# Optimization experiments

Hardware: AMD Instinct MI355X
Metric: run time of the kernel (lower is better)

Reference implementation:

```python
import jax, jax.numpy as jnp
import numpy as np

B, C, H, W = 2, 256, 48, 64
NLVL, NHEAD, D1 = 4, 8, 32


def _avg_pool2(x):
    b, c, h, w = x.shape
    return x.reshape(b, c, h // 2, 2, w // 2, 2).mean(axis=(3, 5))


def _grid_sample(img, grid):
    """Bilinear grid_sample, align_corners=False, zeros padding.
    img: [B,C,Hi,Wi], grid: [B,Hg,Wg,2] in [-1,1]. Returns [B,C,Hg,Wg]."""
    _, _, Hi, Wi = img.shape
    x = (grid[..., 0] + 1.0) * 0.5 * Wi - 0.5
    y = (grid[..., 1] + 1.0) * 0.5 * Hi - 0.5
    x0 = jnp.floor(x)
    y0 = jnp.floor(y)
    wx1 = x - x0
    wx0 = 1.0 - wx1
    wy1 = y - y0
    wy0 = 1.0 - wy1

    def corner(xi, yi, wgt):
        valid = (xi >= 0) & (xi <= Wi - 1) & (yi >= 0) & (yi <= Hi - 1)
        xc = jnp.clip(xi, 0, Wi - 1).astype(jnp.int32)
        yc = jnp.clip(yi, 0, Hi - 1).astype(jnp.int32)
        v = jax.vmap(lambda im, yy, xx: im[:, yy, xx])(img, yc, xc)  # [B,C,Hg,Wg]
        return v * (wgt * valid)[:, None]

    return (corner(x0, y0, wx0 * wy0) + corner(x0 + 1, y0, wx1 * wy0)
            + corner(x0, y0 + 1, wx0 * wy1) + corner(x0 + 1, y0 + 1, wx1 * wy1))


def _forward(fmap1, fmap2, coords, num_levels, num_head):
    batch, _, n1, d1, h1, w1 = coords.shape
    # pyramid from fmap2 (register)
    pyr = [fmap2]
    f2 = fmap2
    for _ in range(num_levels - 1):
        f2 = _avg_pool2(f2)
        pyr.append(f2)
    c = jnp.transpose(coords, (2, 0, 4, 5, 3, 1)).reshape(num_levels, batch, h1 * w1, d1, 2)
    f1 = fmap1[..., None]  # [B,C,h1,w1,1]
    outs = []
    for i in range(num_levels):
        coord = c[i]
        xg = 2.0 * (coord[..., 0] + 0.5) / w1 - 1.0
        yg = 2.0 * (coord[..., 1] + 0.5) / h1 - 1.0
        grid = jnp.stack([xg, yg], axis=-1)  # [B, h1*w1, d1, 2]
        s = _grid_sample(pyr[i], grid)  # [B, C, h1*w1, d1]
        s = s.reshape(batch, -1, h1, w1, d1)
        corr = jnp.abs(f1 - s)  # [B,C,h1,w1,d1]
        corr = corr.reshape(batch, num_head, -1, h1, w1, d1).mean(axis=2)  # [B,nh,h1,w1,d1]
        corr = jnp.transpose(corr, (0, 2, 3, 1, 4)).reshape(batch, h1, w1, -1)
        outs.append(corr)
    out = jnp.concatenate(outs, axis=-1)  # [B,h1,w1,nlvl*nh*d1]
    return jnp.transpose(out, (0, 3, 1, 2)).astype(jnp.float32)


def setup_inputs() -> dict:
    key = jax.random.key(0)
    k1, k2, k3 = jax.random.split(key, 3)
    fmap1 = jax.random.normal(k1, (B, C, H, W), dtype=jnp.float32)
    fmap2 = jax.random.normal(k2, (B, C, H, W), dtype=jnp.float32)
    # coords in fmap1 pixel units: x in [0,W), y in [0,H)
    u = jax.random.uniform(k3, (B, 2, NLVL, D1, H, W), dtype=jnp.float32)
    scale = jnp.array([W, H], dtype=jnp.float32).reshape(1, 2, 1, 1, 1, 1)
    coords = u * scale
    return {"fmap1": fmap1, "fmap2": fmap2, "coords": coords,
            "num_levels": NLVL, "num_head": NHEAD}


def reference(fmap1, fmap2, coords, num_levels, num_head):
    return _forward(fmap1, fmap2, coords, num_levels, num_head)
```

## Files before the change

### kernel.cpp

```cpp
#include <hip/hip_runtime.h>

typedef _Float16 h2 __attribute__((ext_vector_type(2)));

static constexpr int B2   = 2;
static constexpr int C    = 256;
static constexpr int H    = 48;
static constexpr int W    = 64;
static constexpr int NLVL = 4;
static constexpr int D1   = 32;
static constexpr int P    = H * W;
static constexpr int CHO  = NLVL * 8 * D1;

static constexpr size_t F1_BYTES = (size_t)B2 * P * C * 2;
static constexpr size_t PL0 = 0;
static constexpr size_t PL1 = PL0 + (size_t)B2 * 48 * 64 * C;
static constexpr size_t PL2 = PL1 + (size_t)B2 * 24 * 32 * C;
static constexpr size_t PL3 = PL2 + (size_t)B2 * 12 * 16 * C;
static constexpr size_t PYR_BYTES = PL3 + (size_t)B2 * 6 * 8 * C;
static constexpr size_t OT_OFF    = F1_BYTES + PYR_BYTES;
static constexpr size_t OT_BYTES  = (size_t)B2 * P * CHO * 2;
static constexpr size_t WS_NEEDED = OT_OFF + OT_BYTES;

#if defined(__has_builtin)
#if __has_builtin(__builtin_amdgcn_cvt_scalef32_pk_f16_fp8)
#define HAS_HW_FP8_DEC 1
#endif
#if __has_builtin(__builtin_amdgcn_cvt_pk_fp8_f32)
#define HAS_HW_FP8_ENC 1
#endif
#endif

#ifdef HAS_HW_FP8_DEC
static constexpr float WSC = 1.0f;
#else
static constexpr float WSC = 256.0f;
#endif

__device__ __forceinline__ h2 u2h(unsigned u) {
  union { unsigned u; h2 h; } c; c.u = u; return c.h;
}
__device__ __forceinline__ unsigned h2u(h2 h) {
  union { unsigned u; h2 h; } c; c.h = h; return c.u;
}
__device__ __forceinline__ h2 habs2(h2 x) { return u2h(h2u(x) & 0x7FFF7FFFu); }

#ifdef HAS_HW_FP8_ENC
__device__ __forceinline__ unsigned packdw(float a, float b, float c, float d) {
  int v = __builtin_amdgcn_cvt_pk_fp8_f32(a, b, 0, false);
  v = __builtin_amdgcn_cvt_pk_fp8_f32(c, d, v, true);
  return (unsigned)v;
}
#else
__device__ __forceinline__ unsigned f2e4m3(float f) {
  const unsigned b = __float_as_uint(f);
  const unsigned s = (b >> 24) & 0x80u;
  const float a = fabsf(f);
  if (a < 0.015625f) return s;
  if (a >= 448.f) return s | 0x7Eu;
  const unsigned m   = (b >> 20) & 0x7u;
  const unsigned rem = b & 0xFFFFFu;
  const unsigned e32 = (b >> 23) & 0xFFu;
  unsigned v = ((e32 - 120u) << 3) | m;
  if (rem > 0x80000u || (rem == 0x80000u && (v & 1u))) ++v;
  if (v > 0x7Eu) v = 0x7Eu;
  return s | v;
}
__device__ __forceinline__ unsigned packdw(float a, float b, float c, float d) {
  return f2e4m3(a) | (f2e4m3(b) << 8) | (f2e4m3(c) << 16) | (f2e4m3(d) << 24);
}
#endif

#ifndef HAS_HW_FP8_DEC
__device__ __forceinline__ void fp8x4_to_h2x2(unsigned x, h2& lo, h2& hi) {
  const unsigned lo16 = ((x & 0x7Fu) << 7) | ((x & 0x80u) << 8) |
                        ((x & 0x7F00u) << 15) | ((x & 0x8000u) << 16);
  const unsigned y = x >> 16;
  const unsigned hi16 = ((y & 0x7Fu) << 7) | ((y & 0x80u) << 8) |
                        ((y & 0x7F00u) << 15) | ((y & 0x8000u) << 16);
  lo = u2h(lo16); hi = u2h(hi16);
}
#endif

#define PACK8(v, i0) make_uint2(packdw(v[(i0)], v[(i0)+1], v[(i0)+2], v[(i0)+3]), \
                                packdw(v[(i0)+4], v[(i0)+5], v[(i0)+6], v[(i0)+7]))

__global__ __launch_bounds__(256) void k_prep(
    const float* __restrict__ f1, const float* __restrict__ f2,
    char* __restrict__ ws) {
  __shared__ float s0[32][8][16];
  __shared__ float s1[32][4][8];
  __shared__ float s2[32][2][4];
  const int x0 = blockIdx.x * 16;
  const int y0 = blockIdx.y * 8;
  const int z  = blockIdx.z;
  const bool isf1 = (z >= 16);
  const int zb = z & 15;
  const int b  = zb >> 3;
  const int c0 = (zb & 7) * 32;
  const int t  = threadIdx.x;
  const int tx = t & 15, ty = (t >> 4) & 3, tc = t >> 6;

  const float* src = (isf1 ? f1 : f2) + ((size_t)b * C + c0) * P;
#pragma unroll
  for (int k = 0; k < 8; ++k) {
    const int c = tc + 4 * k;
#pragma unroll
    for (int j = 0; j < 2; ++j) {
      const int y = ty + 4 * j;
      s0[c][y][tx] = src[(size_t)c * P + (size_t)(y0 + y) * W + (x0 + tx)];
    }
  }
  __syncthreads();

  char* pyr = ws + F1_BYTES;

  if (t < 128) {
    const int y = t >> 4, x = t & 15;
    float v[32];
#pragma unroll
    for (int e = 0; e < 32; ++e) v[e] = s0[e][y][x];
    if (isf1) {
      union { uint4 q[4]; h2 hh[16]; } u;
#pragma unroll
      for (int e = 0; e < 16; ++e) {
        u.hh[e].x = (_Float16)v[2 * e];
        u.hh[e].y = (_Float16)v[2 * e + 1];
      }
      char* dst = ws + (((size_t)b * P + (size_t)(y0 + y) * W + (x0 + x)) * C + c0) * 2;
#pragma unroll
      for (int q = 0; q < 4; ++q) reinterpret_cast<uint4*>(dst)[q] = u.q[q];
    } else {
      char* dst = pyr + PL0 + ((size_t)b * P + (size_t)(y0 + y) * W + (x0 + x)) * C + c0;
      reinterpret_cast<uint2*>(dst)[0] = PACK8(v, 0);
      reinterpret_cast<uint2*>(dst)[1] = PACK8(v, 8);
      reinterpret_cast<uint2*>(dst)[2] = PACK8(v, 16);
      reinterpret_cast<uint2*>(dst)[3] = PACK8(v, 24);
    }
  } else if (!isf1) {
    const int u0 = t - 128;
#pragma unroll
    for (int k = 0; k < 8; ++k) {
      const int idx = u0 + 128 * k;
      const int c = idx >> 5, r = idx & 31, y = r >> 3, x = r & 7;
      s1[c][y][x] = 0.25f * (s0[c][2 * y][2 * x] + s0[c][2 * y][2 * x + 1] +
                             s0[c][2 * y + 1][2 * x] + s0[c][2 * y + 1][2 * x + 1]);
    }
  }
  if (isf1) return;
  __syncthreads();

  if (t < 32) {
    const int y = t >> 3, x = t & 7;
    float v[32];
#pragma unroll
    for (int e = 0; e < 32; ++e) v[e] = s1[e][y][x];
    char* dst = pyr + PL1 +
                ((size_t)b * (24 * 32) + (size_t)(y0 / 2 + y) * 32 + (x0 / 2 + x)) * C + c0;
    reinterpret_cast<uint2*>(dst)[0] = PACK8(v, 0);
    reinterpret_cast<uint2*>(dst)[1] = PACK8(v, 8);
    reinterpret_cast<uint2*>(dst)[2] = PACK8(v, 16);
    reinterpret_cast<uint2*>(dst)[3] = PACK8(v, 24);
  } else if (t >= 64 && t < 192) {
    const int u0 = t - 64;
#pragma unroll
    for (int k = 0; k < 2; ++k) {
      const int idx = u0 + 128 * k;
      const int c = idx >> 3, r = idx & 7, y = r >> 2, x = r & 3;
      s2[c][y][x] = 0.25f * (s1[c][2 * y][2 * x] + s1[c][2 * y][2 * x + 1] +
                             s1[c][2 * y + 1][2 * x] + s1[c][2 * y + 1][2 * x + 1]);
    }
  }
  __syncthreads();

  if (t < 8) {
    const int y = t >> 2, x = t & 3;
    float v[32];
#pragma unroll
    for (int e = 0; e < 32; ++e) v[e] = s2[e][y][x];
    char* dst = pyr + PL2 +
                ((size_t)b * (12 * 16) + (size_t)(y0 / 4 + y) * 16 + (x0 / 4 + x)) * C + c0;
    reinterpret_cast<uint2*>(dst)[0] = PACK8(v, 0);
    reinterpret_cast<uint2*>(dst)[1] = PACK8(v, 8);
    reinterpret_cast<uint2*>(dst)[2] = PACK8(v, 16);
    reinterpret_cast<uint2*>(dst)[3] = PACK8(v, 24);
  } else if (t >= 8 && t < 10) {
    const int x = t - 8;
    float v[32];
#pragma unroll
    for (int e = 0; e < 32; ++e)
      v[e] = 0.25f * (s2[e][0][2 * x] + s2[e][0][2 * x + 1] +
                      s2[e][1][2 * x] + s2[e][1][2 * x + 1]);
    char* dst = pyr + PL3 +
                ((size_t)b * (6 * 8) + (size_t)(y0 / 8) * 8 + (x0 / 8 + x)) * C + c0;
    reinterpret_cast<uint2*>(dst)[0] = PACK8(v, 0);
    reinterpret_cast<uint2*>(dst)[1] = PACK8(v, 8);
    reinterpret_cast<uint2*>(dst)[2] = PACK8(v, 16);
    reinterpret_cast<uint2*>(dst)[3] = PACK8(v, 24);
  }
}

template <int STAGED>
__global__ __launch_bounds__(256, 4) void k_sample(
    const _Float16* __restrict__ f1cl, const char* __restrict__ pyr,
    const float* __restrict__ coords, float* __restrict__ dstf,
    _Float16* __restrict__ dsth) {
  __shared__ uint4 s_off[128];
  __shared__ uint4 s_w[128];
  __shared__ float s_out[128 * 9];
  const int bid0 = blockIdx.x;
  const int bid  = (bid0 & 7) * 768 + (bid0 >> 3);
  const int b    = (bid >= P) ? 1 : 0;
  const int pix  = bid - b * P;
  const int t    = threadIdx.x;

  if (t < 128) {
    const int lvl = t >> 5, d = t & 31;
    const float cx = coords[(((size_t)(b * 2 + 0) * NLVL + lvl) * D1 + d) * P + pix];
    const float cy = coords[(((size_t)(b * 2 + 1) * NLVL + lvl) * D1 + d) * P + pix];
    const int Hi = H >> lvl, Wi = W >> lvl;
    const float sc = 1.0f / (float)(1 << lvl);
    const float xf = (cx + 0.5f) * sc - 0.5f;
    const float yf = (cy + 0.5f) * sc - 0.5f;
    const float x0f = floorf(xf), y0f = floorf(yf);
    const int x0 = (int)x0f, y0 = (int)y0f;
    const int x1 = x0 + 1, y1 = y0 + 1;
    const float fx = xf - x0f, fy = yf - y0f;
    const float vx0 = (x0 >= 0 && x0 < Wi) ? -WSC : 0.f;
    const float vx1 = (x1 >= 0 && x1 < Wi) ? -WSC : 0.f;
    const float vy0 = (y0 >= 0 && y0 < Hi) ? 1.f : 0.f;
    const float vy1 = (y1 >= 0 && y1 < Hi) ? 1.f : 0.f;
    const int x0c = min(max(x0, 0), Wi - 1), x1c = min(max(x1, 0), Wi - 1);
    const int y0c = min(max(y0, 0), Hi - 1), y1c = min(max(y1, 0), Hi - 1);
    h2 p00, p10, p01, p11;
    p00.x = p00.y = (_Float16)((1.f - fx) * (1.f - fy) * vx0 * vy0);
    p10.x = p10.y = (_Float16)(fx * (1.f - fy) * vx1 * vy0);
    p01.x = p01.y = (_Float16)((1.f - fx) * fy * vx0 * vy1);
    p11.x = p11.y = (_Float16)(fx * fy * vx1 * vy1);
    s_w[t] = make_uint4(h2u(p00), h2u(p10), h2u(p01), h2u(p11));
    const unsigned npx = (unsigned)(Hi * Wi);
    const unsigned lbase =
        (unsigned)((lvl == 0) ? PL0 : (lvl == 1) ? PL1 : (lvl == 2) ? PL2 : PL3) +
        (unsigned)b * npx * C;
    s_off[t] = make_uint4(lbase + (unsigned)(y0c * Wi + x0c) * C,
                          lbase + (unsigned)(y0c * Wi + x1c) * C,
                          lbase + (unsigned)(y1c * Wi + x0c) * C,
                          lbase + (unsigned)(y1c * Wi + x1c) * C);
  }

  const int lane = t & 63;
  const int wave = t >> 6;
  const int q    = lane >> 4;
  const int li   = lane & 15;
  const unsigned chb = (unsigned)li * 16u;

  h2 f1h[8];
  {
    const uint4* fp = reinterpret_cast<const uint4*>(
        reinterpret_cast<const char*>(f1cl) + ((size_t)b * P + pix) * (C * 2) + li * 32);
    const uint4 fa = fp[0], fb = fp[1];
    f1h[0] = u2h(fa.x); f1h[1] = u2h(fa.y); f1h[2] = u2h(fa.z); f1h[3] = u2h(fa.w);
    f1h[4] = u2h(fb.x); f1h[5] = u2h(fb.y); f1h[6] = u2h(fb.z); f1h[7] = u2h(fb.w);
  }

  __syncthreads();

#ifdef HAS_HW_FP8_DEC
#define DECFMA(v, wu)                                                          \
  {                                                                            \
    const h2 w = u2h(wu);                                                      \
    acc[0] += w * __builtin_amdgcn_cvt_scalef32_pk_f16_fp8((v).x, 1.0f, false);\
    acc[1] += w * __builtin_amdgcn_cvt_scalef32_pk_f16_fp8((v).x, 1.0f, true); \
    acc[2] += w * __builtin_amdgcn_cvt_scalef32_pk_f16_fp8((v).y, 1.0f, false);\
    acc[3] += w * __builtin_amdgcn_cvt_scalef32_pk_f16_fp8((v).y, 1.0f, true); \
    acc[4] += w * __builtin_amdgcn_cvt_scalef32_pk_f16_fp8((v).z, 1.0f, false);\
    acc[5] += w * __builtin_amdgcn_cvt_scalef32_pk_f16_fp8((v).z, 1.0f, true); \
    acc[6] += w * __builtin_amdgcn_cvt_scalef32_pk_f16_fp8((v).w, 1.0f, false);\
    acc[7] += w * __builtin_amdgcn_cvt_scalef32_pk_f16_fp8((v).w, 1.0f, true); \
  }
#else
#define DECFMA(v, wu)                                                          \
  {                                                                            \
    const h2 w = u2h(wu);                                                      \
    h2 lo, hi;                                                                 \
    fp8x4_to_h2x2((v).x, lo, hi); acc[0] += w * lo; acc[1] += w * hi;          \
    fp8x4_to_h2x2((v).y, lo, hi); acc[2] += w * lo; acc[3] += w * hi;          \
    fp8x4_to_h2x2((v).z, lo, hi); acc[4] += w * lo; acc[5] += w * hi;          \
    fp8x4_to_h2x2((v).w, lo, hi); acc[6] += w * lo; acc[7] += w * hi;          \
  }
#endif

#define REDUCE_STORE(sidx)                                                     \
  {                                                                            \
    const h2 s01 = habs2(acc[0]) + habs2(acc[1]);                              \
    const h2 s23 = habs2(acc[2]) + habs2(acc[3]);                              \
    const h2 s45 = habs2(acc[4]) + habs2(acc[5]);                              \
    const h2 s67 = habs2(acc[6]) + habs2(acc[7]);                              \
    const h2 s   = (s01 + s23) + (s45 + s67);                                  \
    float a = (float)s.x + (float)s.y;                                         \
    a += __shfl_xor(a, 1);                                                     \
    if ((li & 1) == 0) s_out[(sidx) * 9 + (li >> 1)] = a * (1.0f / 32.0f);     \
  }

#pragma unroll
  for (int ip = 0; ip < 4; ++ip) {
    const int sA = (2 * ip) * 16 + wave * 4 + q;
    const int sB = sA + 16;
    const uint4 oA = s_off[sA], wA = s_w[sA];
    const uint4 oB = s_off[sB], wB = s_w[sB];
    const uint4 a0 = *reinterpret_cast<const uint4*>(pyr + (oA.x + chb));
    const uint4 a1 = *reinterpret_cast<const uint4*>(pyr + (oA.y + chb));
    const uint4 a2 = *reinterpret_cast<const uint4*>(pyr + (oA.z + chb));
    const uint4 a3 = *reinterpret_cast<const uint4*>(pyr + (oA.w + chb));
    const uint4 b0 = *reinterpret_cast<const uint4*>(pyr + (oB.x + chb));
    const uint4 b1 = *reinterpret_cast<const uint4*>(pyr + (oB.y + chb));
    const uint4 b2 = *reinterpret_cast<const uint4*>(pyr + (oB.z + chb));
    const uint4 b3 = *reinterpret_cast<const uint4*>(pyr + (oB.w + chb));
    {
      h2 acc[8];
#pragma unroll
      for (int k = 0; k < 8; ++k) acc[k] = f1h[k];
      DECFMA(a0, wA.x) DECFMA(a1, wA.y) DECFMA(a2, wA.z) DECFMA(a3, wA.w)
      REDUCE_STORE(sA)
    }
    {
      h2 acc[8];
#pragma unroll
      for (int k = 0; k < 8; ++k) acc[k] = f1h[k];
      DECFMA(b0, wB.x) DECFMA(b1, wB.y) DECFMA(b2, wB.z) DECFMA(b3, wB.w)
      REDUCE_STORE(sB)
    }
  }

  __syncthreads();
  if (STAGED) {
    union { unsigned qq[2]; h2 hh[2]; } u;
#pragma unroll
    for (int j = 0; j < 2; ++j) {
      const int c0i = t * 4 + j * 2;
      const int c1i = c0i + 1;
      u.hh[j].x = (_Float16)s_out[((c0i >> 8) * 32 + (c0i & 31)) * 9 + ((c0i >> 5) & 7)];
      u.hh[j].y = (_Float16)s_out[((c1i >> 8) * 32 + (c1i & 31)) * 9 + ((c1i >> 5) & 7)];
    }
    *reinterpret_cast<uint2*>(dsth + ((size_t)b * P + pix) * CHO + t * 4) =
        make_uint2(u.qq[0], u.qq[1]);
  } else {
#pragma unroll
    for (int j = 0; j < 4; ++j) {
      const int ch = t * 4 + j;
      dstf[((size_t)b * CHO + ch) * P + pix] =
          s_out[((ch >> 8) * 32 + (ch & 31)) * 9 + ((ch >> 5) & 7)];
    }
  }
}

__global__ __launch_bounds__(256) void k_out_t(
    const _Float16* __restrict__ ot, float* __restrict__ out) {
  __shared__ float tile[32][33];
  const int b  = blockIdx.z;
  const int p0 = blockIdx.x * 32;
  const int c0 = blockIdx.y * 32;
  const int tx = threadIdx.x, ty = threadIdx.y;
#pragma unroll
  for (int i = 0; i < 32; i += 8)
    tile[ty + i][tx] = (float)ot[((size_t)b * P + p0 + ty + i) * CHO + c0 + tx];
  __syncthreads();
#pragma unroll
  for (int i = 0; i < 32; i += 8)
    out[((size_t)b * CHO + c0 + ty + i) * P + p0 + tx] = tile[tx][ty + i];
}

extern "C" void kernel_launch(void* const* d_in, const int* in_sizes, int n_in,
                              void* d_out, int out_size, void* d_ws, size_t ws_size,
                              hipStream_t stream) {
  const float* fmap1  = (const float*)d_in[0];
  const float* fmap2  = (const float*)d_in[1];
  const float* coords = (const float*)d_in[2];
  float* out = (float*)d_out;
  char* ws   = (char*)d_ws;

  k_prep<<<dim3(4, 6, 32), 256, 0, stream>>>(fmap1, fmap2, ws);

  const _Float16* f1cl = (const _Float16*)ws;
  const char* pyr = ws + F1_BYTES;
  if (ws_size >= WS_NEEDED) {
    _Float16* ot = (_Float16*)(ws + OT_OFF);
    k_sample<1><<<B2 * P, 256, 0, stream>>>(f1cl, pyr, coords, out, ot);
    k_out_t<<<dim3(96, 32, 2), dim3(32, 8), 0, stream>>>(ot, out);
  } else {
    k_sample<0><<<B2 * P, 256, 0, stream>>>(f1cl, pyr, coords, out, nullptr);
  }
}
```

Baseline: 57.92 us.

## Fuse output transpose into sampler with 8-pixel strips per block

The sampling kernel now processes a strip of 8 consecutive pixels per 512-thread block, one wave per pixel. Results are staged in shared memory as half precision and written directly in channel-major layout with float4 stores. This removes the intermediate fp16 workspace buffer and the separate transpose kernel launch. In exchange it uses much more shared memory per block and launches fewer, larger blocks, which may lower occupancy and latency hiding for the gather loads.

```diff
diff --git a/kernel.cpp b/kernel.cpp
--- a/kernel.cpp
+++ b/kernel.cpp
@@ -17,9 +17,6 @@
 static constexpr size_t PL2 = PL1 + (size_t)B2 * 24 * 32 * C;
 static constexpr size_t PL3 = PL2 + (size_t)B2 * 12 * 16 * C;
 static constexpr size_t PYR_BYTES = PL3 + (size_t)B2 * 6 * 8 * C;
-static constexpr size_t OT_OFF    = F1_BYTES + PYR_BYTES;
-static constexpr size_t OT_BYTES  = (size_t)B2 * P * CHO * 2;
-static constexpr size_t WS_NEEDED = OT_OFF + OT_BYTES;
 
 #if defined(__has_builtin)
 #if __has_builtin(__builtin_amdgcn_cvt_scalef32_pk_f16_fp8)
@@ -199,22 +196,26 @@
   }
 }
 
-template <int STAGED>
-__global__ __launch_bounds__(256, 4) void k_sample(
+__global__ __launch_bounds__(512, 4) void k_sample(
     const _Float16* __restrict__ f1cl, const char* __restrict__ pyr,
-    const float* __restrict__ coords, float* __restrict__ dstf,
-    _Float16* __restrict__ dsth) {
-  __shared__ uint4 s_off[128];
-  __shared__ uint4 s_w[128];
-  __shared__ float s_out[128 * 9];
-  const int bid0 = blockIdx.x;
-  const int bid  = (bid0 & 7) * 768 + (bid0 >> 3);
-  const int b    = (bid >= P) ? 1 : 0;
-  const int pix  = bid - b * P;
-  const int t    = threadIdx.x;
-
-  if (t < 128) {
-    const int lvl = t >> 5, d = t & 31;
+    const float* __restrict__ coords, float* __restrict__ out) {
+  __shared__ uint4 s_off[8 * 128];
+  __shared__ uint4 s_w[8 * 128];
+  __shared__ _Float16 s_out[8 * 1024];
+  const int bid0  = blockIdx.x;
+  const int bid   = (bid0 & 7) * 96 + (bid0 >> 3);
+  const int b     = bid / 384;
+  const int strip = bid - b * 384;
+  const int pix0  = strip * 8;
+  const int t     = threadIdx.x;
+
+#pragma unroll
+  for (int i = 0; i < 2; ++i) {
+    const int idx  = i * 512 + t;
+    const int px   = idx & 7;
+    const int slot = idx >> 3;
+    const int lvl  = slot >> 5, d = slot & 31;
+    const int pix  = pix0 + px;
     const float cx = coords[(((size_t)(b * 2 + 0) * NLVL + lvl) * D1 + d) * P + pix];
     const float cy = coords[(((size_t)(b * 2 + 1) * NLVL + lvl) * D1 + d) * P + pix];
     const int Hi = H >> lvl, Wi = W >> lvl;
@@ -236,15 +237,15 @@
     p10.x = p10.y = (_Float16)(fx * (1.f - fy) * vx1 * vy0);
     p01.x = p01.y = (_Float16)((1.f - fx) * fy * vx0 * vy1);
     p11.x = p11.y = (_Float16)(fx * fy * vx1 * vy1);
-    s_w[t] = make_uint4(h2u(p00), h2u(p10), h2u(p01), h2u(p11));
+    s_w[px * 128 + slot] = make_uint4(h2u(p00), h2u(p10), h2u(p01), h2u(p11));
     const unsigned npx = (unsigned)(Hi * Wi);
     const unsigned lbase =
         (unsigned)((lvl == 0) ? PL0 : (lvl == 1) ? PL1 : (lvl == 2) ? PL2 : PL3) +
         (unsigned)b * npx * C;
-    s_off[t] = make_uint4(lbase + (unsigned)(y0c * Wi + x0c) * C,
-                          lbase + (unsigned)(y0c * Wi + x1c) * C,
-                          lbase + (unsigned)(y1c * Wi + x0c) * C,
-                          lbase + (unsigned)(y1c * Wi + x1c) * C);
+    s_off[px * 128 + slot] = make_uint4(lbase + (unsigned)(y0c * Wi + x0c) * C,
+                                        lbase + (unsigned)(y0c * Wi + x1c) * C,
+                                        lbase + (unsigned)(y1c * Wi + x0c) * C,
+                                        lbase + (unsigned)(y1c * Wi + x1c) * C);
   }
 
   const int lane = t & 63;
@@ -252,6 +253,7 @@
   const int q    = lane >> 4;
   const int li   = lane & 15;
   const unsigned chb = (unsigned)li * 16u;
+  const int pix  = pix0 + wave;
 
   h2 f1h[8];
   {
@@ -289,84 +291,48 @@
   }
 #endif
 
-#define REDUCE_STORE(sidx)                                                     \
-  {                                                                            \
-    const h2 s01 = habs2(acc[0]) + habs2(acc[1]);                              \
-    const h2 s23 = habs2(acc[2]) + habs2(acc[3]);                              \
-    const h2 s45 = habs2(acc[4]) + habs2(acc[5]);                              \
-    const h2 s67 = habs2(acc[6]) + habs2(acc[7]);                              \
-    const h2 s   = (s01 + s23) + (s45 + s67);                                  \
-    float a = (float)s.x + (float)s.y;                                         \
-    a += __shfl_xor(a, 1);                                                     \
-    if ((li & 1) == 0) s_out[(sidx) * 9 + (li >> 1)] = a * (1.0f / 32.0f);     \
-  }
-
-#pragma unroll
-  for (int ip = 0; ip < 4; ++ip) {
-    const int sA = (2 * ip) * 16 + wave * 4 + q;
-    const int sB = sA + 16;
-    const uint4 oA = s_off[sA], wA = s_w[sA];
-    const uint4 oB = s_off[sB], wB = s_w[sB];
-    const uint4 a0 = *reinterpret_cast<const uint4*>(pyr + (oA.x + chb));
-    const uint4 a1 = *reinterpret_cast<const uint4*>(pyr + (oA.y + chb));
-    const uint4 a2 = *reinterpret_cast<const uint4*>(pyr + (oA.z + chb));
-    const uint4 a3 = *reinterpret_cast<const uint4*>(pyr + (oA.w + chb));
-    const uint4 b0 = *reinterpret_cast<const uint4*>(pyr + (oB.x + chb));
-    const uint4 b1 = *reinterpret_cast<const uint4*>(pyr + (oB.y + chb));
-    const uint4 b2 = *reinterpret_cast<const uint4*>(pyr + (oB.z + chb));
-    const uint4 b3 = *reinterpret_cast<const uint4*>(pyr + (oB.w + chb));
-    {
-      h2 acc[8];
-#pragma unroll
-      for (int k = 0; k < 8; ++k) acc[k] = f1h[k];
-      DECFMA(a0, wA.x) DECFMA(a1, wA.y) DECFMA(a2, wA.z) DECFMA(a3, wA.w)
-      REDUCE_STORE(sA)
-    }
-    {
-      h2 acc[8];
-#pragma unroll
-      for (int k = 0; k < 8; ++k) acc[k] = f1h[k];
-      DECFMA(b0, wB.x) DECFMA(b1, wB.y) DECFMA(b2, wB.z) DECFMA(b3, wB.w)
-      REDUCE_STORE(sB)
-    }
-  }
-
-  __syncthreads();
-  if (STAGED) {
-    union { unsigned qq[2]; h2 hh[2]; } u;
-#pragma unroll
-    for (int j = 0; j < 2; ++j) {
-      const int c0i = t * 4 + j * 2;
-      const int c1i = c0i + 1;
-      u.hh[j].x = (_Float16)s_out[((c0i >> 8) * 32 + (c0i & 31)) * 9 + ((c0i >> 5) & 7)];
-      u.hh[j].y = (_Float16)s_out[((c1i >> 8) * 32 + (c1i & 31)) * 9 + ((c1i >> 5) & 7)];
-    }
-    *reinterpret_cast<uint2*>(dsth + ((size_t)b * P + pix) * CHO + t * 4) =
-        make_uint2(u.qq[0], u.qq[1]);
-  } else {
-#pragma unroll
-    for (int j = 0; j < 4; ++j) {
-      const int ch = t * 4 + j;
-      dstf[((size_t)b * CHO + ch) * P + pix] =
-          s_out[((ch >> 8) * 32 + (ch & 31)) * 9 + ((ch >> 5) & 7)];
-    }
-  }
-}
-
-__global__ __launch_bounds__(256) void k_out_t(
-    const _Float16* __restrict__ ot, float* __restrict__ out) {
-  __shared__ float tile[32][33];
-  const int b  = blockIdx.z;
-  const int p0 = blockIdx.x * 32;
-  const int c0 = blockIdx.y * 32;
-  const int tx = threadIdx.x, ty = threadIdx.y;
-#pragma unroll
-  for (int i = 0; i < 32; i += 8)
-    tile[ty + i][tx] = (float)ot[((size_t)b * P + p0 + ty + i) * CHO + c0 + tx];
-  __syncthreads();
-#pragma unroll
-  for (int i = 0; i < 32; i += 8)
-    out[((size_t)b * CHO + c0 + ty + i) * P + p0 + tx] = tile[tx][ty + i];
+  const uint4* soff = &s_off[wave * 128];
+  const uint4* swgt = &s_w[wave * 128];
+  _Float16* sout    = &s_out[wave * 1024];
+
+#pragma unroll 4
+  for (int p = 0; p < 32; ++p) {
+    const int slot = p * 4 + q;
+    const uint4 o  = soff[slot];
+    const uint4 wq = swgt[slot];
+    const uint4 v0 = *reinterpret_cast<const uint4*>(pyr + (o.x + chb));
+    const uint4 v1 = *reinterpret_cast<const uint4*>(pyr + (o.y + chb));
+    const uint4 v2 = *reinterpret_cast<const uint4*>(pyr + (o.z + chb));
+    const uint4 v3 = *reinterpret_cast<const uint4*>(pyr + (o.w + chb));
+    h2 acc[8];
+#pragma unroll
+    for (int k = 0; k < 8; ++k) acc[k] = f1h[k];
+    DECFMA(v0, wq.x) DECFMA(v1, wq.y) DECFMA(v2, wq.z) DECFMA(v3, wq.w)
+    const h2 s01 = habs2(acc[0]) + habs2(acc[1]);
+    const h2 s23 = habs2(acc[2]) + habs2(acc[3]);
+    const h2 s45 = habs2(acc[4]) + habs2(acc[5]);
+    const h2 s67 = habs2(acc[6]) + habs2(acc[7]);
+    const h2 s   = (s01 + s23) + (s45 + s67);
+    float a = (float)s.x + (float)s.y;
+    a += __shfl_xor(a, 1);
+    if ((li & 1) == 0) {
+      const int ch_out = (slot >> 5) * 256 + (li >> 1) * 32 + (slot & 31);
+      sout[ch_out] = (_Float16)(a * (1.0f / 32.0f));
+    }
+  }
+
+  __syncthreads();
+
+#pragma unroll
+  for (int cc = 0; cc < 2; ++cc) {
+    const int ch = cc * 512 + t;
+    float v[8];
+#pragma unroll
+    for (int px = 0; px < 8; ++px) v[px] = (float)s_out[px * 1024 + ch];
+    float4* dp = reinterpret_cast<float4*>(out + ((size_t)b * CHO + ch) * P + pix0);
+    dp[0] = make_float4(v[0], v[1], v[2], v[3]);
+    dp[1] = make_float4(v[4], v[5], v[6], v[7]);
+  }
 }
 
 extern "C" void kernel_launch(void* const* d_in, const int* in_sizes, int n_in,
@@ -382,11 +348,5 @@
 
   const _Float16* f1cl = (const _Float16*)ws;
   const char* pyr = ws + F1_BYTES;
-  if (ws_size >= WS_NEEDED) {
-    _Float16* ot = (_Float16*)(ws + OT_OFF);
-    k_sample<1><<<B2 * P, 256, 0, stream>>>(f1cl, pyr, coords, out, ot);
-    k_out_t<<<dim3(96, 32, 2), dim3(32, 8), 0, stream>>>(ot, out);
-  } else {
-    k_sample<0><<<B2 * P, 256, 0, stream>>>(f1cl, pyr, coords, out, nullptr);
-  }
-}
+  k_sample<<<768, 512, 0, stream>>>(f1cl, pyr, coords, out);
+}
```

New measurement: 61.08 us. +5.5%, slower.
